# Performance work log

Measured on AMD Instinct MI355X. Metric: run time of the kernel, lower is better.

## Reference

```python
import jax, jax.numpy as jnp
import numpy as np

B, T, D, H, W = 2, 8192, 512, 8, 256
d = D // H  # 64
NC = T // W  # number of chunks (T divisible by W)


def setup_inputs() -> dict:
    key = jax.random.key(0)
    ks = jax.random.split(key, 9)
    s = 1.0 / np.sqrt(D).astype(np.float32)
    x = jax.random.normal(ks[0], (B, T, D), jnp.float32)
    Wq = jax.random.normal(ks[1], (D, D), jnp.float32) * s
    Wk = jax.random.normal(ks[2], (D, D), jnp.float32) * s
    Wv = jax.random.normal(ks[3], (D, D), jnp.float32) * s
    Wo = jax.random.normal(ks[4], (D, D), jnp.float32) * s
    bq = jax.random.normal(ks[5], (D,), jnp.float32) * 0.01
    bk = jax.random.normal(ks[6], (D,), jnp.float32) * 0.01
    bv = jax.random.normal(ks[7], (D,), jnp.float32) * 0.01
    bo = jax.random.normal(ks[8], (D,), jnp.float32) * 0.01
    return {"x": x, "Wq": Wq, "bq": bq, "Wk": Wk, "bk": bk,
            "Wv": Wv, "bv": bv, "Wo": Wo, "bo": bo}


def _local_attention(q, k, v):
    # q, k, v: [B, H, T, d]. Each W-sized query chunk attends to keys in
    # [chunk_start - W, chunk_end + W) -> a 3W window, masked at boundaries.
    qc = q.reshape(B, H, NC, W, d)
    pad = ((0, 0), (0, 0), (W, W), (0, 0))
    kp = jnp.pad(k, pad)
    vp = jnp.pad(v, pad)
    # window gather indices into padded sequence: [NC, 3W]
    pos = jnp.arange(NC)[:, None] * W + jnp.arange(3 * W)[None, :]
    kw = kp[:, :, pos, :]  # [B, H, NC, 3W, d]
    vw = vp[:, :, pos, :]  # [B, H, NC, 3W, d]
    valid = (pos >= W) & (pos < T + W)  # [NC, 3W] true for real (unpadded) keys
    scores = jnp.einsum('bhcqd,bhckd->bhcqk', qc, kw) * (d ** -0.5)
    scores = jnp.where(valid[None, None, :, None, :], scores, -jnp.inf)
    attn = jax.nn.softmax(scores, axis=-1)
    out = jnp.einsum('bhcqk,bhckd->bhcqd', attn, vw)
    return out.reshape(B, H, T, d)


def reference(x, Wq, bq, Wk, bk, Wv, bv, Wo, bo):
    # Linear = x @ W.T + b (torch nn.Linear convention)
    q = (x @ Wq.T + bq).reshape(B, T, H, d).transpose(0, 2, 1, 3)
    # k_proj / v_proj run under torch.no_grad() in the original
    k = jax.lax.stop_gradient(x @ Wk.T + bk).reshape(B, T, H, d).transpose(0, 2, 1, 3)
    v = jax.lax.stop_gradient(x @ Wv.T + bv).reshape(B, T, H, d).transpose(0, 2, 1, 3)
    out = _local_attention(q, k, v)           # [B, H, T, d]
    out = out.transpose(0, 2, 1, 3).reshape(B, T, D)
    return out @ Wo.T + bo
```

## Files before the change

kernel.cpp:

```cpp
#include <hip/hip_runtime.h>
#include <hip/hip_bf16.h>

typedef unsigned short u16;
typedef unsigned int   u32;
typedef __bf16 bf16x8 __attribute__((ext_vector_type(8)));
typedef float  f32x4  __attribute__((ext_vector_type(4)));

#define BB 2
#define TT 8192
#define DD 512
#define HH 8
#define WW 256
#define DH 64
#define NX 8388608
#define NW 262144

__device__ __forceinline__ float b2f(u16 u) {
    unsigned int x = ((unsigned int)u) << 16;
    return __builtin_bit_cast(float, x);
}
__device__ __forceinline__ u16 f2b(float f) {
    __bf16 h = (__bf16)f;
    return __builtin_bit_cast(u16, h);
}
__device__ __forceinline__ bf16x8 ldsfrag(const u16* p) {
    return *(const bf16x8*)p;
}
__device__ __forceinline__ f32x4 mfma16(bf16x8 a, bf16x8 b, f32x4 c) {
    return __builtin_amdgcn_mfma_f32_16x16x32_bf16(a, b, c, 0, 0, 0);
}

typedef __attribute__((address_space(1))) u32 gu32;
typedef __attribute__((address_space(3))) u32 lu32;
__device__ __forceinline__ void gl_lds(const u16* g, u16* l) {
    __builtin_amdgcn_global_load_lds((gu32*)g, (lu32*)l, 16, 0, 0);
}

__device__ __forceinline__ void cvt8(const void* s, u16* d, long i, int f) {
    if (f) {
        const u32* sp = (const u32*)s + i;
        uint4 a = *(const uint4*)(sp);
        uint4 b = *(const uint4*)(sp + 4);
        u16 o[8];
        o[0] = f2b(__builtin_bit_cast(float, a.x));
        o[1] = f2b(__builtin_bit_cast(float, a.y));
        o[2] = f2b(__builtin_bit_cast(float, a.z));
        o[3] = f2b(__builtin_bit_cast(float, a.w));
        o[4] = f2b(__builtin_bit_cast(float, b.x));
        o[5] = f2b(__builtin_bit_cast(float, b.y));
        o[6] = f2b(__builtin_bit_cast(float, b.z));
        o[7] = f2b(__builtin_bit_cast(float, b.w));
        *(uint4*)(d + i) = *(const uint4*)o;
    } else {
        *(uint4*)(d + i) = *(const uint4*)((const u16*)s + i);
    }
}

__global__ void convert_all(const void* x, const void* Wq, const void* bq,
                            const void* Wk, const void* bk, const void* Wv,
                            const void* bv, const void* Wo, const void* bo,
                            u16* __restrict__ xb, u16* __restrict__ Wcat,
                            u16* __restrict__ Wob, u16* __restrict__ bcat,
                            u16* __restrict__ bob, int* __restrict__ flagw)
{
    __shared__ int sflag;
    const int tid = threadIdx.x;
    if (tid == 0) sflag = 0;
    __syncthreads();
    int mybad = 0;
    for (int i = tid; i < 2048; i += 256) {
        float v = b2f(((const u16*)x)[i]);
        if (!(fabsf(v) < 100.f)) mybad = 1;
    }
    if (mybad) atomicOr(&sflag, 1);
    __syncthreads();
    const int f = sflag ? 1 : 0;
    if (blockIdx.x == 0 && tid == 0) *flagw = f;

    long i = ((long)blockIdx.x * 256 + tid) * 8;
    if (i < NX)            { if (f) cvt8(x, xb, i, f); return; }
    i -= NX;
    if (i < NW)            { cvt8(Wq, Wcat,         i, f); return; }
    i -= NW;
    if (i < NW)            { cvt8(Wk, Wcat + NW,    i, f); return; }
    i -= NW;
    if (i < NW)            { cvt8(Wv, Wcat + 2*NW,  i, f); return; }
    i -= NW;
    if (i < NW)            { cvt8(Wo, Wob,          i, f); return; }
    i -= NW;
    if (i < 512)           { cvt8(bq, bcat,         i, f); return; }
    i -= 512;
    if (i < 512)           { cvt8(bk, bcat + 512,   i, f); return; }
    i -= 512;
    if (i < 512)           { cvt8(bv, bcat + 1024,  i, f); return; }
    i -= 512;
    if (i < 512)           { cvt8(bo, bob,          i, f); }
}

__global__ __launch_bounds__(256, 2)
void gemm128(const u16* __restrict__ A, const u16* __restrict__ Aalt,
             const u16* __restrict__ Bw, const u16* __restrict__ bias,
             void* __restrict__ out0, u16* __restrict__ out1,
             u16* __restrict__ out2, int mode, const int* __restrict__ flagp)
{
    __shared__ __align__(16) u16 AsF[128 * 64];
    __shared__ __align__(16) u16 BsF[128 * 64];

    const int tid  = threadIdx.x;
    const int lane = tid & 63;
    const int wv   = tid >> 6;
    const int col  = lane & 15;
    const int quad = lane >> 4;
    const int wm   = (wv & 1) * 64;
    const int wn   = (wv >> 1) * 64;
    const int m0   = blockIdx.x * 128;
    const int n0   = blockIdx.y * 128;

    const int f = *flagp;
    const u16* Ap = f ? A : Aalt;

    const bool swapped = (mode == 1) || (blockIdx.y < 8);

    f32x4 acc[4][4] = {};

    for (int k0 = 0; k0 < 512; k0 += 64) {
        __syncthreads();
        #pragma unroll
        for (int i = 0; i < 4; i++) {
            const int r  = (wv * 4 + i) * 8 + (lane >> 3);
            const int cb = (lane & 7) ^ (r & 7);
            gl_lds(Ap + (size_t)(m0 + r) * 512 + k0 + cb * 8, &AsF[(wv * 4 + i) * 512]);
            gl_lds(Bw + (size_t)(n0 + r) * 512 + k0 + cb * 8, &BsF[(wv * 4 + i) * 512]);
        }
        __syncthreads();
        #pragma unroll
        for (int kk = 0; kk < 2; kk++) {
            bf16x8 fx[4], fw[4];
            #pragma unroll
            for (int mi = 0; mi < 4; mi++)
                fx[mi] = ldsfrag(&AsF[(wm + mi * 16 + col) * 64 + ((kk * 4 + quad) ^ (col & 7)) * 8]);
            #pragma unroll
            for (int ni = 0; ni < 4; ni++)
                fw[ni] = ldsfrag(&BsF[(wn + ni * 16 + col) * 64 + ((kk * 4 + quad) ^ (col & 7)) * 8]);
            if (swapped) {
                #pragma unroll
                for (int ni = 0; ni < 4; ni++)
                    #pragma unroll
                    for (int mi = 0; mi < 4; mi++)
                        acc[ni][mi] = mfma16(fw[ni], fx[mi], acc[ni][mi]);
            } else {
                #pragma unroll
                for (int mi = 0; mi < 4; mi++)
                    #pragma unroll
                    for (int ni = 0; ni < 4; ni++)
                        acc[mi][ni] = mfma16(fx[mi], fw[ni], acc[mi][ni]);
            }
        }
    }

    if (swapped) {
        const int outf32 = (mode == 1) && f;
        #pragma unroll
        for (int mi = 0; mi < 4; mi++) {
            const int gm = m0 + wm + mi * 16 + col;
            #pragma unroll
            for (int ni = 0; ni < 4; ni++) {
                const int gn = n0 + wn + ni * 16 + quad * 4;
                uint2 bv2 = *(const uint2*)(bias + gn);
                const u16* bp = (const u16*)&bv2;
                float v[4];
                #pragma unroll
                for (int r = 0; r < 4; r++) v[r] = acc[ni][mi][r] + b2f(bp[r]);
                if (mode == 1) {
                    if (outf32) {
                        uint4 pk;
                        pk.x = __builtin_bit_cast(u32, v[0]);
                        pk.y = __builtin_bit_cast(u32, v[1]);
                        pk.z = __builtin_bit_cast(u32, v[2]);
                        pk.w = __builtin_bit_cast(u32, v[3]);
                        *(uint4*)&((float*)out0)[(size_t)gm * 512 + gn] = pk;
                    } else {
                        uint2 pk;
                        pk.x = f2b(v[0]) | ((u32)f2b(v[1]) << 16);
                        pk.y = f2b(v[2]) | ((u32)f2b(v[3]) << 16);
                        *(uint2*)&((u16*)out0)[(size_t)gm * 512 + gn] = pk;
                    }
                } else {
                    u16* dst = (gn < 512) ? (u16*)out0 : out1;
                    uint2 pk;
                    pk.x = f2b(v[0]) | ((u32)f2b(v[1]) << 16);
                    pk.y = f2b(v[2]) | ((u32)f2b(v[3]) << 16);
                    *(uint2*)&dst[(size_t)gm * 512 + (gn & 511)] = pk;
                }
            }
        }
    } else {
        #pragma unroll
        for (int ni = 0; ni < 4; ni++) {
            const int gn = n0 + wn + ni * 16 + col;
            const float bv = b2f(bias[gn]);
            const int d = gn & 63, hh = (gn >> 6) & 7;
            #pragma unroll
            for (int mi = 0; mi < 4; mi++) {
                const int gmb = m0 + wm + mi * 16 + quad * 4;
                const int bb = gmb >> 13, t = gmb & 8191;
                u16 pb[4];
                #pragma unroll
                for (int r = 0; r < 4; r++) pb[r] = f2b(acc[mi][ni][r] + bv);
                uint2 pk;
                pk.x = pb[0] | ((u32)pb[1] << 16);
                pk.y = pb[2] | ((u32)pb[3] << 16);
                *(uint2*)&out2[((size_t)(bb * 8 + hh) * 64 + d) * 8192 + t] = pk;
            }
        }
    }
}

#define PSW 72
__global__ __launch_bounds__(512, 4)
void attn_local(const u16* __restrict__ Qg, const u16* __restrict__ Kg,
                const u16* __restrict__ VTg, u16* __restrict__ Og)
{
    __shared__ __align__(16) u16 Ks[2][64 * 64];
    __shared__ __align__(16) u16 VTs[2][64 * 64];
    __shared__ __align__(16) u16 Ps[8][32 * PSW];

    const int tid  = threadIdx.x;
    const int lane = tid & 63;
    const int wv   = tid >> 6;
    const int col  = lane & 15;
    const int quad = lane >> 4;

    const int idx = blockIdx.x;
    const int c = idx & 31;
    const int h = (idx >> 5) & 7;
    const int b = idx >> 8;

    const int t0 = c * WW;
    const int wq = wv * 32;

    const int sc_lo = (c == 0) ? 4 : 0;
    const int nsc   = (c == 0 || c == 31) ? 8 : 12;

    const int ldr = lane >> 3;
    const int ldc = lane & 7;

    bf16x8 qf[2][2];
    {
        const size_t qbase = ((size_t)(b * TT + t0 + wq + col)) * DD + h * DH + quad * 8;
        #pragma unroll
        for (int qi = 0; qi < 2; qi++)
            #pragma unroll
            for (int kk = 0; kk < 2; kk++)
                qf[qi][kk] = *(const bf16x8*)(Qg + qbase + (size_t)qi * 16 * DD + kk * 32);
    }

    f32x4 o[4][2] = {};
    float lsum[2] = {0.f, 0.f};

    u16* psb = &Ps[wv][0];

    {
        const int kstart = t0 - WW + sc_lo * 64;
        const int rr = wv * 8 + ldr;
        const int cb = ldc ^ (rr & 7);
        gl_lds(Kg  + ((size_t)(b * TT + kstart + rr)) * DD + h * DH + cb * 8,
               &Ks[0][wv * 512]);
        gl_lds(VTg + ((size_t)((b * HH + h) * DH + rr)) * TT + kstart + cb * 8,
               &VTs[0][wv * 512]);
    }

    for (int it = 0; it < nsc; it++) {
        __syncthreads();
        if (it + 1 < nsc) {
            const int kstart = t0 - WW + (sc_lo + it + 1) * 64;
            const int buf = (it + 1) & 1;
            const int rr = wv * 8 + ldr;
            const int cb = ldc ^ (rr & 7);
            gl_lds(Kg  + ((size_t)(b * TT + kstart + rr)) * DD + h * DH + cb * 8,
                   &Ks[buf][wv * 512]);
            gl_lds(VTg + ((size_t)((b * HH + h) * DH + rr)) * TT + kstart + cb * 8,
                   &VTs[buf][wv * 512]);
        }
        const u16* ks = &Ks[it & 1][0];
        const u16* vs = &VTs[it & 1][0];

        f32x4 s[4][2];
        #pragma unroll
        for (int ns = 0; ns < 4; ns++)
            #pragma unroll
            for (int qi = 0; qi < 2; qi++)
                s[ns][qi] = (f32x4){0.f, 0.f, 0.f, 0.f};
        #pragma unroll
        for (int ns = 0; ns < 4; ns++) {
            const int row = ns * 16 + col;
            bf16x8 ka0 = ldsfrag(&ks[row * 64 + ((0 + quad) ^ (col & 7)) * 8]);
            bf16x8 ka1 = ldsfrag(&ks[row * 64 + ((4 + quad) ^ (col & 7)) * 8]);
            #pragma unroll
            for (int qi = 0; qi < 2; qi++) {
                s[ns][qi] = mfma16(ka0, qf[qi][0], s[ns][qi]);
                s[ns][qi] = mfma16(ka1, qf[qi][1], s[ns][qi]);
            }
        }

        #pragma unroll
        for (int ns = 0; ns < 4; ns++) {
            #pragma unroll
            for (int qi = 0; qi < 2; qi++) {
                u16 pb[4];
                #pragma unroll
                for (int r = 0; r < 4; r++) {
                    const float p = __expf(s[ns][qi][r] * 0.125f);
                    pb[r] = f2b(p);
                    lsum[qi] += p;
                }
                uint2 pk;
                pk.x = pb[0] | ((u32)pb[1] << 16);
                pk.y = pb[2] | ((u32)pb[3] << 16);
                *(uint2*)&psb[(qi * 16 + col) * PSW + ns * 16 + quad * 4] = pk;
            }
        }
        asm volatile("" ::: "memory");

        #pragma unroll
        for (int kt = 0; kt < 2; kt++) {
            bf16x8 pf[2];
            #pragma unroll
            for (int qi = 0; qi < 2; qi++)
                pf[qi] = ldsfrag(&psb[(qi * 16 + col) * PSW + kt * 32 + quad * 8]);
            #pragma unroll
            for (int di = 0; di < 4; di++) {
                bf16x8 va = ldsfrag(&vs[(di * 16 + col) * 64 + ((kt * 4 + quad) ^ (col & 7)) * 8]);
                #pragma unroll
                for (int qi = 0; qi < 2; qi++)
                    o[di][qi] = mfma16(va, pf[qi], o[di][qi]);
            }
        }
    }

    #pragma unroll
    for (int qi = 0; qi < 2; qi++) {
        float l = lsum[qi];
        l += __shfl_xor(l, 16);
        l += __shfl_xor(l, 32);
        lsum[qi] = 1.0f / l;
    }

    #pragma unroll
    for (int qi = 0; qi < 2; qi++) {
        const size_t ob = ((size_t)(b * TT + t0 + wq + qi * 16 + col)) * DD + h * DH + quad * 4;
        #pragma unroll
        for (int di = 0; di < 4; di++) {
            u16 pb[4];
            #pragma unroll
            for (int r = 0; r < 4; r++) pb[r] = f2b(o[di][qi][r] * lsum[qi]);
            uint2 pk;
            pk.x = pb[0] | ((u32)pb[1] << 16);
            pk.y = pb[2] | ((u32)pb[3] << 16);
            *(uint2*)&Og[ob + di * 16] = pk;
        }
    }
}

extern "C" void kernel_launch(void* const* d_in, const int* in_sizes, int n_in,
                              void* d_out, int out_size, void* d_ws, size_t ws_size,
                              hipStream_t stream)
{
    u16* ws   = (u16*)d_ws;
    u16* xb   = ws;
    u16* Wcat = xb + NX;
    u16* Wob  = Wcat + 3 * NW;
    u16* bcat = Wob + NW;
    u16* bob  = bcat + 1536;
    u16* qws  = bob + 512;
    u16* kws  = qws + NX;
    u16* vtws = kws + NX;
    u16* aws  = vtws + NX;
    int* flag = (int*)(aws + NX);

    convert_all<<<4609, 256, 0, stream>>>(
        d_in[0], d_in[1], d_in[2], d_in[3], d_in[4], d_in[5], d_in[6], d_in[7], d_in[8],
        xb, Wcat, Wob, bcat, bob, flag);

    gemm128<<<dim3(128, 12), 256, 0, stream>>>(
        xb, (const u16*)d_in[0], Wcat, bcat, qws, kws, vtws, 0, flag);
    attn_local<<<dim3(BB * HH * 32), 512, 0, stream>>>(qws, kws, vtws, aws);
    gemm128<<<dim3(128, 4), 256, 0, stream>>>(
        aws, aws, Wob, bob, d_out, nullptr, nullptr, 1, flag);
}
```

Measured before the change: 195.2 us.

## Keep softmax probabilities in registers, split GEMMs, skip bf16 weight copies

```diff
diff --git a/kernel.cpp b/kernel.cpp
--- a/kernel.cpp
+++ b/kernel.cpp
@@ -4,6 +4,8 @@
 typedef unsigned short u16;
 typedef unsigned int   u32;
 typedef __bf16 bf16x8 __attribute__((ext_vector_type(8)));
+typedef __bf16 bf16x4 __attribute__((ext_vector_type(4)));
+typedef short  s16x4  __attribute__((ext_vector_type(4)));
 typedef float  f32x4  __attribute__((ext_vector_type(4)));
 
 #define BB 2
@@ -30,30 +32,48 @@
     return __builtin_amdgcn_mfma_f32_16x16x32_bf16(a, b, c, 0, 0, 0);
 }
 
+#if defined(__has_builtin)
+#if __has_builtin(__builtin_amdgcn_mfma_f32_16x16x16_bf16)
+__device__ __forceinline__ f32x4 mfma16k(bf16x4 a, bf16x4 b, f32x4 c) {
+    return __builtin_amdgcn_mfma_f32_16x16x16_bf16(a, b, c, 0, 0, 0);
+}
+#define HAVE_MFMA16K 1
+#elif __has_builtin(__builtin_amdgcn_mfma_f32_16x16x16bf16_1k)
+__device__ __forceinline__ f32x4 mfma16k(bf16x4 a, bf16x4 b, f32x4 c) {
+    return __builtin_amdgcn_mfma_f32_16x16x16bf16_1k(
+        __builtin_bit_cast(s16x4, a), __builtin_bit_cast(s16x4, b), c, 0, 0, 0);
+}
+#define HAVE_MFMA16K 1
+#endif
+#endif
+#ifndef HAVE_MFMA16K
+__device__ __forceinline__ f32x4 mfma16k(bf16x4 a, bf16x4 b, f32x4 c) {
+    bf16x8 a8 = {a[0], a[1], a[2], a[3], (__bf16)0.f, (__bf16)0.f, (__bf16)0.f, (__bf16)0.f};
+    bf16x8 b8 = {b[0], b[1], b[2], b[3], (__bf16)0.f, (__bf16)0.f, (__bf16)0.f, (__bf16)0.f};
+    return __builtin_amdgcn_mfma_f32_16x16x32_bf16(a8, b8, c, 0, 0, 0);
+}
+#endif
+
 typedef __attribute__((address_space(1))) u32 gu32;
 typedef __attribute__((address_space(3))) u32 lu32;
 __device__ __forceinline__ void gl_lds(const u16* g, u16* l) {
     __builtin_amdgcn_global_load_lds((gu32*)g, (lu32*)l, 16, 0, 0);
 }
 
-__device__ __forceinline__ void cvt8(const void* s, u16* d, long i, int f) {
-    if (f) {
-        const u32* sp = (const u32*)s + i;
-        uint4 a = *(const uint4*)(sp);
-        uint4 b = *(const uint4*)(sp + 4);
-        u16 o[8];
-        o[0] = f2b(__builtin_bit_cast(float, a.x));
-        o[1] = f2b(__builtin_bit_cast(float, a.y));
-        o[2] = f2b(__builtin_bit_cast(float, a.z));
-        o[3] = f2b(__builtin_bit_cast(float, a.w));
-        o[4] = f2b(__builtin_bit_cast(float, b.x));
-        o[5] = f2b(__builtin_bit_cast(float, b.y));
-        o[6] = f2b(__builtin_bit_cast(float, b.z));
-        o[7] = f2b(__builtin_bit_cast(float, b.w));
-        *(uint4*)(d + i) = *(const uint4*)o;
-    } else {
-        *(uint4*)(d + i) = *(const uint4*)((const u16*)s + i);
-    }
+__device__ __forceinline__ void cvt8(const void* s, u16* d, long i) {
+    const u32* sp = (const u32*)s + i;
+    uint4 a = *(const uint4*)(sp);
+    uint4 b = *(const uint4*)(sp + 4);
+    u16 o[8];
+    o[0] = f2b(__builtin_bit_cast(float, a.x));
+    o[1] = f2b(__builtin_bit_cast(float, a.y));
+    o[2] = f2b(__builtin_bit_cast(float, a.z));
+    o[3] = f2b(__builtin_bit_cast(float, a.w));
+    o[4] = f2b(__builtin_bit_cast(float, b.x));
+    o[5] = f2b(__builtin_bit_cast(float, b.y));
+    o[6] = f2b(__builtin_bit_cast(float, b.z));
+    o[7] = f2b(__builtin_bit_cast(float, b.w));
+    *(uint4*)(d + i) = *(const uint4*)o;
 }
 
 __global__ void convert_all(const void* x, const void* Wq, const void* bq,
@@ -76,32 +96,38 @@
     __syncthreads();
     const int f = sflag ? 1 : 0;
     if (blockIdx.x == 0 && tid == 0) *flagw = f;
+    if (!f) return;
 
     long i = ((long)blockIdx.x * 256 + tid) * 8;
-    if (i < NX)            { if (f) cvt8(x, xb, i, f); return; }
+    if (i < NX)            { cvt8(x,  xb,           i); return; }
     i -= NX;
-    if (i < NW)            { cvt8(Wq, Wcat,         i, f); return; }
+    if (i < NW)            { cvt8(Wq, Wcat,         i); return; }
     i -= NW;
-    if (i < NW)            { cvt8(Wk, Wcat + NW,    i, f); return; }
+    if (i < NW)            { cvt8(Wk, Wcat + NW,    i); return; }
     i -= NW;
-    if (i < NW)            { cvt8(Wv, Wcat + 2*NW,  i, f); return; }
+    if (i < NW)            { cvt8(Wv, Wcat + 2*NW,  i); return; }
     i -= NW;
-    if (i < NW)            { cvt8(Wo, Wob,          i, f); return; }
+    if (i < NW)            { cvt8(Wo, Wob,          i); return; }
     i -= NW;
-    if (i < 512)           { cvt8(bq, bcat,         i, f); return; }
+    if (i < 512)           { cvt8(bq, bcat,         i); return; }
     i -= 512;
-    if (i < 512)           { cvt8(bk, bcat + 512,   i, f); return; }
+    if (i < 512)           { cvt8(bk, bcat + 512,   i); return; }
     i -= 512;
-    if (i < 512)           { cvt8(bv, bcat + 1024,  i, f); return; }
+    if (i < 512)           { cvt8(bv, bcat + 1024,  i); return; }
     i -= 512;
-    if (i < 512)           { cvt8(bo, bob,          i, f); }
+    if (i < 512)           { cvt8(bo, bob,          i); }
 }
 
 __global__ __launch_bounds__(256, 2)
-void gemm128(const u16* __restrict__ A, const u16* __restrict__ Aalt,
-             const u16* __restrict__ Bw, const u16* __restrict__ bias,
-             void* __restrict__ out0, u16* __restrict__ out1,
-             u16* __restrict__ out2, int mode, const int* __restrict__ flagp)
+void gemm_qkv(const u16* __restrict__ xcvt, const u16* __restrict__ xraw,
+              const u16* __restrict__ Wcat,
+              const u16* __restrict__ Wqr, const u16* __restrict__ Wkr,
+              const u16* __restrict__ Wvr,
+              const u16* __restrict__ bcat,
+              const u16* __restrict__ bqr, const u16* __restrict__ bkr,
+              const u16* __restrict__ bvr,
+              u16* __restrict__ outQ, u16* __restrict__ outK,
+              u16* __restrict__ outVT, const int* __restrict__ flagp)
 {
     __shared__ __align__(16) u16 AsF[128 * 64];
     __shared__ __align__(16) u16 BsF[128 * 64];
@@ -114,12 +140,18 @@
     const int wm   = (wv & 1) * 64;
     const int wn   = (wv >> 1) * 64;
     const int m0   = blockIdx.x * 128;
-    const int n0   = blockIdx.y * 128;
-
-    const int f = *flagp;
-    const u16* Ap = f ? A : Aalt;
-
-    const bool swapped = (mode == 1) || (blockIdx.y < 8);
+
+    const int f    = *flagp;
+    const int seg  = blockIdx.y >> 2;
+    const int nl0  = (blockIdx.y & 3) * 128;
+
+    const u16* Ap = f ? xcvt : xraw;
+    const u16* Bp = f ? (Wcat + (size_t)seg * NW)
+                      : (seg == 0 ? Wqr : (seg == 1 ? Wkr : Wvr));
+    const u16* bp = f ? (bcat + seg * 512)
+                      : (seg == 0 ? bqr : (seg == 1 ? bkr : bvr));
+
+    const bool swapped = (seg < 2);
 
     f32x4 acc[4][4] = {};
 
@@ -130,7 +162,7 @@
             const int r  = (wv * 4 + i) * 8 + (lane >> 3);
             const int cb = (lane & 7) ^ (r & 7);
             gl_lds(Ap + (size_t)(m0 + r) * 512 + k0 + cb * 8, &AsF[(wv * 4 + i) * 512]);
-            gl_lds(Bw + (size_t)(n0 + r) * 512 + k0 + cb * 8, &BsF[(wv * 4 + i) * 512]);
+            gl_lds(Bp + (size_t)(nl0 + r) * 512 + k0 + cb * 8, &BsF[(wv * 4 + i) * 512]);
         }
         __syncthreads();
         #pragma unroll
@@ -159,47 +191,29 @@
     }
 
     if (swapped) {
-        const int outf32 = (mode == 1) && f;
+        u16* dst = (seg == 0) ? outQ : outK;
         #pragma unroll
         for (int mi = 0; mi < 4; mi++) {
             const int gm = m0 + wm + mi * 16 + col;
             #pragma unroll
             for (int ni = 0; ni < 4; ni++) {
-                const int gn = n0 + wn + ni * 16 + quad * 4;
-                uint2 bv2 = *(const uint2*)(bias + gn);
-                const u16* bp = (const u16*)&bv2;
-                float v[4];
-                #pragma unroll
-                for (int r = 0; r < 4; r++) v[r] = acc[ni][mi][r] + b2f(bp[r]);
-                if (mode == 1) {
-                    if (outf32) {
-                        uint4 pk;
-                        pk.x = __builtin_bit_cast(u32, v[0]);
-                        pk.y = __builtin_bit_cast(u32, v[1]);
-                        pk.z = __builtin_bit_cast(u32, v[2]);
-                        pk.w = __builtin_bit_cast(u32, v[3]);
-                        *(uint4*)&((float*)out0)[(size_t)gm * 512 + gn] = pk;
-                    } else {
-                        uint2 pk;
-                        pk.x = f2b(v[0]) | ((u32)f2b(v[1]) << 16);
-                        pk.y = f2b(v[2]) | ((u32)f2b(v[3]) << 16);
-                        *(uint2*)&((u16*)out0)[(size_t)gm * 512 + gn] = pk;
-                    }
-                } else {
-                    u16* dst = (gn < 512) ? (u16*)out0 : out1;
-                    uint2 pk;
-                    pk.x = f2b(v[0]) | ((u32)f2b(v[1]) << 16);
-                    pk.y = f2b(v[2]) | ((u32)f2b(v[3]) << 16);
-                    *(uint2*)&dst[(size_t)gm * 512 + (gn & 511)] = pk;
-                }
+                const int gn = nl0 + wn + ni * 16 + quad * 4;
+                uint2 bv2 = *(const uint2*)(bp + gn);
+                const u16* bb = (const u16*)&bv2;
+                uint2 pk;
+                pk.x = f2b(acc[ni][mi][0] + b2f(bb[0])) |
+                       ((u32)f2b(acc[ni][mi][1] + b2f(bb[1])) << 16);
+                pk.y = f2b(acc[ni][mi][2] + b2f(bb[2])) |
+                       ((u32)f2b(acc[ni][mi][3] + b2f(bb[3])) << 16);
+                *(uint2*)&dst[(size_t)gm * 512 + gn] = pk;
             }
         }
     } else {
         #pragma unroll
         for (int ni = 0; ni < 4; ni++) {
-            const int gn = n0 + wn + ni * 16 + col;
-            const float bv = b2f(bias[gn]);
-            const int d = gn & 63, hh = (gn >> 6) & 7;
+            const int gn = nl0 + wn + ni * 16 + col;
+            const float bv = b2f(bp[gn]);
+            const int d = gn & 63, hh = gn >> 6;
             #pragma unroll
             for (int mi = 0; mi < 4; mi++) {
                 const int gmb = m0 + wm + mi * 16 + quad * 4;
@@ -210,20 +224,103 @@
                 uint2 pk;
                 pk.x = pb[0] | ((u32)pb[1] << 16);
                 pk.y = pb[2] | ((u32)pb[3] << 16);
-                *(uint2*)&out2[((size_t)(bb * 8 + hh) * 64 + d) * 8192 + t] = pk;
-            }
-        }
-    }
-}
-
-#define PSW 72
+                *(uint2*)&outVT[((size_t)(bb * 8 + hh) * 64 + d) * 8192 + t] = pk;
+            }
+        }
+    }
+}
+
+__global__ __launch_bounds__(256, 2)
+void gemm_oproj(const u16* __restrict__ A, const u16* __restrict__ Wob,
+                const u16* __restrict__ Wor, const u16* __restrict__ bob,
+                const u16* __restrict__ bor, void* __restrict__ out,
+                const int* __restrict__ flagp)
+{
+    __shared__ __align__(16) u16 AsF[128 * 64];
+    __shared__ __align__(16) u16 BsF[64 * 64];
+
+    const int tid  = threadIdx.x;
+    const int lane = tid & 63;
+    const int wv   = tid >> 6;
+    const int col  = lane & 15;
+    const int quad = lane >> 4;
+    const int wm   = (wv & 1) * 64;
+    const int wn   = (wv >> 1) * 32;
+    const int m0   = blockIdx.x * 128;
+    const int n0   = blockIdx.y * 64;
+
+    const int f = *flagp;
+    const u16* Bp = f ? Wob : Wor;
+    const u16* bp = f ? bob : bor;
+
+    f32x4 acc[2][4] = {};
+
+    for (int k0 = 0; k0 < 512; k0 += 64) {
+        __syncthreads();
+        #pragma unroll
+        for (int i = 0; i < 4; i++) {
+            const int r  = (wv * 4 + i) * 8 + (lane >> 3);
+            const int cb = (lane & 7) ^ (r & 7);
+            gl_lds(A + (size_t)(m0 + r) * 512 + k0 + cb * 8, &AsF[(wv * 4 + i) * 512]);
+        }
+        #pragma unroll
+        for (int i = 0; i < 2; i++) {
+            const int r  = (wv * 2 + i) * 8 + (lane >> 3);
+            const int cb = (lane & 7) ^ (r & 7);
+            gl_lds(Bp + (size_t)(n0 + r) * 512 + k0 + cb * 8, &BsF[(wv * 2 + i) * 512]);
+        }
+        __syncthreads();
+        #pragma unroll
+        for (int kk = 0; kk < 2; kk++) {
+            bf16x8 fx[4], fw[2];
+            #pragma unroll
+            for (int mi = 0; mi < 4; mi++)
+                fx[mi] = ldsfrag(&AsF[(wm + mi * 16 + col) * 64 + ((kk * 4 + quad) ^ (col & 7)) * 8]);
+            #pragma unroll
+            for (int ni = 0; ni < 2; ni++)
+                fw[ni] = ldsfrag(&BsF[(wn + ni * 16 + col) * 64 + ((kk * 4 + quad) ^ (col & 7)) * 8]);
+            #pragma unroll
+            for (int ni = 0; ni < 2; ni++)
+                #pragma unroll
+                for (int mi = 0; mi < 4; mi++)
+                    acc[ni][mi] = mfma16(fw[ni], fx[mi], acc[ni][mi]);
+        }
+    }
+
+    #pragma unroll
+    for (int mi = 0; mi < 4; mi++) {
+        const int gm = m0 + wm + mi * 16 + col;
+        #pragma unroll
+        for (int ni = 0; ni < 2; ni++) {
+            const int gn = n0 + wn + ni * 16 + quad * 4;
+            uint2 bv2 = *(const uint2*)(bp + gn);
+            const u16* bb = (const u16*)&bv2;
+            float v[4];
+            #pragma unroll
+            for (int r = 0; r < 4; r++) v[r] = acc[ni][mi][r] + b2f(bb[r]);
+            if (f) {
+                uint4 pk;
+                pk.x = __builtin_bit_cast(u32, v[0]);
+                pk.y = __builtin_bit_cast(u32, v[1]);
+                pk.z = __builtin_bit_cast(u32, v[2]);
+                pk.w = __builtin_bit_cast(u32, v[3]);
+                *(uint4*)&((float*)out)[(size_t)gm * 512 + gn] = pk;
+            } else {
+                uint2 pk;
+                pk.x = f2b(v[0]) | ((u32)f2b(v[1]) << 16);
+                pk.y = f2b(v[2]) | ((u32)f2b(v[3]) << 16);
+                *(uint2*)&((u16*)out)[(size_t)gm * 512 + gn] = pk;
+            }
+        }
+    }
+}
+
 __global__ __launch_bounds__(512, 4)
 void attn_local(const u16* __restrict__ Qg, const u16* __restrict__ Kg,
                 const u16* __restrict__ VTg, u16* __restrict__ Og)
 {
     __shared__ __align__(16) u16 Ks[2][64 * 64];
     __shared__ __align__(16) u16 VTs[2][64 * 64];
-    __shared__ __align__(16) u16 Ps[8][32 * PSW];
 
     const int tid  = threadIdx.x;
     const int lane = tid & 63;
@@ -257,8 +354,6 @@
 
     f32x4 o[4][2] = {};
     float lsum[2] = {0.f, 0.f};
-
-    u16* psb = &Ps[wv][0];
 
     {
         const int kstart = t0 - WW + sc_lo * 64;
@@ -303,37 +398,33 @@
             }
         }
 
+        bf16x4 pfrag[4][2];
         #pragma unroll
         for (int ns = 0; ns < 4; ns++) {
             #pragma unroll
             for (int qi = 0; qi < 2; qi++) {
-                u16 pb[4];
+                bf16x4 pv;
                 #pragma unroll
                 for (int r = 0; r < 4; r++) {
                     const float p = __expf(s[ns][qi][r] * 0.125f);
-                    pb[r] = f2b(p);
+                    pv[r] = (__bf16)p;
                     lsum[qi] += p;
                 }
-                uint2 pk;
-                pk.x = pb[0] | ((u32)pb[1] << 16);
-                pk.y = pb[2] | ((u32)pb[3] << 16);
-                *(uint2*)&psb[(qi * 16 + col) * PSW + ns * 16 + quad * 4] = pk;
-            }
-        }
-        asm volatile("" ::: "memory");
-
-        #pragma unroll
-        for (int kt = 0; kt < 2; kt++) {
-            bf16x8 pf[2];
-            #pragma unroll
-            for (int qi = 0; qi < 2; qi++)
-                pf[qi] = ldsfrag(&psb[(qi * 16 + col) * PSW + kt * 32 + quad * 8]);
+                pfrag[ns][qi] = pv;
+            }
+        }
+
+        #pragma unroll
+        for (int ns = 0; ns < 4; ns++) {
             #pragma unroll
             for (int di = 0; di < 4; di++) {
-                bf16x8 va = ldsfrag(&vs[(di * 16 + col) * 64 + ((kt * 4 + quad) ^ (col & 7)) * 8]);
+                const u16* vp = vs + (di * 16 + col) * 64
+                              + (((ns * 2 + (quad >> 1)) ^ (col & 7)) * 8)
+                              + (quad & 1) * 4;
+                bf16x4 va = *(const bf16x4*)vp;
                 #pragma unroll
                 for (int qi = 0; qi < 2; qi++)
-                    o[di][qi] = mfma16(va, pf[qi], o[di][qi]);
+                    o[di][qi] = mfma16k(va, pfrag[ns][qi], o[di][qi]);
             }
         }
     }
@@ -382,9 +473,14 @@
         d_in[0], d_in[1], d_in[2], d_in[3], d_in[4], d_in[5], d_in[6], d_in[7], d_in[8],
         xb, Wcat, Wob, bcat, bob, flag);
 
-    gemm128<<<dim3(128, 12), 256, 0, stream>>>(
-        xb, (const u16*)d_in[0], Wcat, bcat, qws, kws, vtws, 0, flag);
+    gemm_qkv<<<dim3(128, 12), 256, 0, stream>>>(
+        xb, (const u16*)d_in[0], Wcat,
+        (const u16*)d_in[1], (const u16*)d_in[3], (const u16*)d_in[5],
+        bcat, (const u16*)d_in[2], (const u16*)d_in[4], (const u16*)d_in[6],
+        qws, kws, vtws, flag);
+
     attn_local<<<dim3(BB * HH * 32), 512, 0, stream>>>(qws, kws, vtws, aws);
-    gemm128<<<dim3(128, 4), 256, 0, stream>>>(
-        aws, aws, Wob, bob, d_out, nullptr, nullptr, 1, flag);
-}
+
+    gemm_oproj<<<dim3(128, 8), 256, 0, stream>>>(
+        aws, Wob, (const u16*)d_in[7], bob, (const u16*)d_in[8], d_out, flag);
+}
```

New measurement: 201.6 us. 1.03x slower.
